# Kernel optimization log

Hardware: AMD Instinct MI355X
Metric: run time of the kernel (lower is better)

## Reference

```python
import jax, jax.numpy as jnp
import numpy as np

NUM_NODES = 16384
NUM_EDGES = 131072
NUM_MOLS = 512
H = 256          # hidden_dim
L = 3            # num_hidden_layers
NUM_RBF = 50
CUTOFF = 5.0
IN_DIM = 5
D_IN = IN_DIM + 3  # atom_types + spherical coords


def setup_inputs() -> dict:
    ks = jax.random.split(jax.random.key(0), 32)
    n = lambda k, s: jax.random.normal(k, s, dtype=jnp.float32) * 0.05
    return {
        "atom_types": jax.random.uniform(ks[0], (NUM_NODES, IN_DIM), dtype=jnp.float32),
        "coords_spherical": jax.random.normal(ks[1], (NUM_NODES, 3), dtype=jnp.float32),
        "edge_dist": jax.random.uniform(ks[2], (NUM_EDGES,), dtype=jnp.float32) * CUTOFF,
        "edge_index": jax.random.randint(ks[3], (2, NUM_EDGES), 0, NUM_NODES, dtype=jnp.int32),
        "node2mol": jnp.arange(NUM_NODES, dtype=jnp.int32) // (NUM_NODES // NUM_MOLS),
        "emb_Wm": n(ks[4], (D_IN, H)), "emb_bm": jnp.zeros((H,), jnp.float32),
        "emb_Wp": n(ks[5], (D_IN, H)), "emb_bp": jnp.zeros((H,), jnp.float32),
        "attn_Wqm": n(ks[6], (L, H, H)), "attn_Wkm": n(ks[7], (L, H, H)), "attn_Wvm": n(ks[8], (L, H, H)),
        "attn_Wqp": n(ks[9], (L, H, H)), "attn_Wkp": n(ks[10], (L, H, H)), "attn_Wvp": n(ks[11], (L, H, H)),
        "attn_We": n(ks[12], (L, NUM_RBF)), "attn_be": jnp.zeros((L,), jnp.float32),
        "mp_We": n(ks[13], (L, NUM_RBF, H)), "mp_be": jnp.zeros((L, H), jnp.float32),
        "mp_Wm": n(ks[14], (L, H, H)), "mp_bm": jnp.zeros((L, H), jnp.float32),
        "mp_Wp": n(ks[15], (L, H, H)), "mp_bp": jnp.zeros((L, H), jnp.float32),
        "ln_g": jnp.ones((L, H), jnp.float32), "ln_b": jnp.zeros((L, H), jnp.float32),
        "proj_W": n(ks[16], (H, H)), "proj_b": jnp.zeros((H,), jnp.float32),
        "head_W1": n(ks[17], (2 * H, H)), "head_b1": jnp.zeros((H,), jnp.float32),
        "head_W2": n(ks[18], (H, H // 2)), "head_b2": jnp.zeros((H // 2,), jnp.float32),
        "head_W3": n(ks[19], (H // 2, 1)), "head_b3": jnp.zeros((1,), jnp.float32),
    }


def _seg_softmax(s, seg, n):
    m = jax.ops.segment_max(s, seg, num_segments=n)
    e = jnp.exp(s - m[seg])
    z = jax.ops.segment_sum(e, seg, num_segments=n)
    return e / (z[seg] + 1e-9)


def _layernorm(x, g, b):
    mu = x.mean(-1, keepdims=True)
    v = ((x - mu) ** 2).mean(-1, keepdims=True)
    return (x - mu) * jax.lax.rsqrt(v + 1e-5) * g + b


def _forward(atom_types, coords_spherical, edge_dist,
             emb_Wm, emb_bm, emb_Wp, emb_bp,
             attn_Wqm, attn_Wkm, attn_Wvm, attn_Wqp, attn_Wkp, attn_Wvp, attn_We, attn_be,
             mp_We, mp_be, mp_Wm, mp_bm, mp_Wp, mp_bp,
             ln_g, ln_b, proj_W, proj_b,
             head_W1, head_b1, head_W2, head_b2, head_W3, head_b3,
             edge_index, node2mol):
    src, dst = edge_index[0], edge_index[1]
    N = NUM_NODES

    # --- RBF expansion (Schutt 2018): 50 gaussians on [0, cutoff] * cosine cutoff ---
    centers = jnp.linspace(0.0, CUTOFF, NUM_RBF)
    delta = CUTOFF / NUM_RBF
    env = 0.5 * (jnp.cos(jnp.pi * edge_dist / CUTOFF) + 1.0) * (edge_dist < CUTOFF)
    rbf = jnp.exp(-0.5 * ((edge_dist[:, None] - centers) / delta) ** 2) * env[:, None]  # [E, R]

    # --- Complex polar embedding ---
    x = jnp.concatenate([atom_types, coords_spherical], axis=-1)  # [N, 8]
    mag = jax.nn.softplus(x @ emb_Wm + emb_bm)
    ph = jnp.pi * jnp.tanh(x @ emb_Wp + emb_bp)

    for l in range(L):
        # --- Complex polar attention: |q||k| cos(phi_q - phi_k), edge bias from rbf ---
        qm, km, vm = mag @ attn_Wqm[l], mag @ attn_Wkm[l], mag @ attn_Wvm[l]
        qp, kp, vp = ph @ attn_Wqp[l], ph @ attn_Wkp[l], ph @ attn_Wvp[l]
        score = jnp.sum(qm[dst] * km[src] * jnp.cos(qp[dst] - kp[src]), axis=-1) / jnp.sqrt(float(H))
        score = score + rbf @ attn_We[l] + attn_be[l]          # [E]
        alpha = _seg_softmax(score, dst, N)                    # [E]
        new_mag = jax.ops.segment_sum(alpha[:, None] * vm[src], dst, num_segments=N)
        new_ph = jax.ops.segment_sum(alpha[:, None] * vp[src], dst, num_segments=N)

        # --- Complex message passing gated by RBF profile ---
        gate = jax.nn.silu(rbf @ mp_We[l] + mp_be[l])          # [E, H]
        agg_m = jax.ops.segment_sum(gate * new_mag[src], dst, num_segments=N)
        agg_p = jax.ops.segment_sum(gate * new_ph[src], dst, num_segments=N)
        new_mag = new_mag + agg_m @ mp_Wm[l] + mp_bm[l]
        new_ph = new_ph + agg_p @ mp_Wp[l] + mp_bp[l]

        # --- residual + LayerNorm on magnitude (dropout = identity at eval) ---
        new_mag = new_mag + mag
        new_ph = new_ph + ph
        mag = _layernorm(new_mag, ln_g[l], ln_b[l])
        ph = new_ph

    # --- real projection + dual (mean, sum) pooling per molecule ---
    atom_repr = (mag * jnp.cos(ph)) @ proj_W + proj_b          # [N, H]
    s = jax.ops.segment_sum(atom_repr, node2mol, num_segments=NUM_MOLS)
    cnt = jax.ops.segment_sum(jnp.ones((N, 1), atom_repr.dtype), node2mol, num_segments=NUM_MOLS)
    mol = jnp.concatenate([s / jnp.maximum(cnt, 1.0), s], axis=-1)  # [B, 2H]

    h = jax.nn.silu(mol @ head_W1 + head_b1)
    h = jax.nn.silu(h @ head_W2 + head_b2)
    return h @ head_W3 + head_b3                               # [B, 1]


def reference(atom_types, coords_spherical, edge_dist,
              emb_Wm, emb_bm, emb_Wp, emb_bp,
              attn_Wqm, attn_Wkm, attn_Wvm, attn_Wqp, attn_Wkp, attn_Wvp, attn_We, attn_be,
              mp_We, mp_be, mp_Wm, mp_bm, mp_Wp, mp_bp,
              ln_g, ln_b, proj_W, proj_b,
              head_W1, head_b1, head_W2, head_b2, head_W3, head_b3,
              edge_index, node2mol):
    return _forward(atom_types, coords_spherical, edge_dist,
                    emb_Wm, emb_bm, emb_Wp, emb_bp,
                    attn_Wqm, attn_Wkm, attn_Wvm, attn_Wqp, attn_Wkp, attn_Wvp, attn_We, attn_be,
                    mp_We, mp_be, mp_Wm, mp_bm, mp_Wp, mp_bp,
                    ln_g, ln_b, proj_W, proj_b,
                    head_W1, head_b1, head_W2, head_b2, head_W3, head_b3,
                    edge_index, node2mol)
```

## Files before the change

### kernel.cpp

```cpp
#include <hip/hip_runtime.h>
#include <math.h>

#define N_NODES 16384
#define N_EDGES 131072
#define N_MOLS 512
#define HDIM 256
#define NLAYER 3
#define NRBF 50
#define CUT 5.0f
#define HH (HDIM*HDIM)

typedef unsigned short u16;
typedef __attribute__((ext_vector_type(8))) short short8v;
typedef __attribute__((ext_vector_type(4))) float f32x4;
typedef __attribute__((ext_vector_type(4))) unsigned short u16x4;
typedef __attribute__((ext_vector_type(8))) unsigned short u16x8;
typedef __attribute__((ext_vector_type(2))) unsigned short u16x2;

__device__ __forceinline__ float softplusf(float x){ return fmaxf(x,0.f)+log1pf(expf(-fabsf(x))); }
__device__ __forceinline__ float siluf(float x){ return x/(1.f+expf(-x)); }
__device__ __forceinline__ float bf2f(u16 u){ union{unsigned int i; float f;}v; v.i=((unsigned int)u)<<16; return v.f; }
__device__ __forceinline__ u16 f2bf(float f){ union{float f; unsigned int i;}v; v.f=f; unsigned int r = v.i + 0x7FFFu + ((v.i>>16)&1u); return (u16)(r>>16); }

__device__ __forceinline__ void gload_lds16(const void* g, void* l){
  __builtin_amdgcn_global_load_lds((const __attribute__((address_space(1))) unsigned int*)g,
                                   (__attribute__((address_space(3))) unsigned int*)l, 16, 0, 0);
}

__global__ void k_hist(const int* __restrict__ dst, int* __restrict__ cnt){
  int e = blockIdx.x*256 + threadIdx.x;
  if(e < N_EDGES) atomicAdd(&cnt[dst[e]], 1);
}

__global__ __launch_bounds__(1024) void k_scan(const int* __restrict__ cnt,
                                               int* __restrict__ rowptr,
                                               int* __restrict__ cursor){
  __shared__ int part[1024];
  int tid = threadIdx.x;
  int base = tid*16;
  int loc[16]; int s=0;
  #pragma unroll
  for(int i=0;i<16;i++){ loc[i]=s; s+=cnt[base+i]; }
  part[tid]=s; __syncthreads();
  for(int off=1; off<1024; off<<=1){
    int v = (tid>=off)? part[tid-off] : 0;
    __syncthreads();
    part[tid] += v;
    __syncthreads();
  }
  int pre = (tid==0)?0:part[tid-1];
  #pragma unroll
  for(int i=0;i<16;i++){ int v = pre+loc[i]; rowptr[base+i]=v; cursor[base+i]=v; }
  if(tid==1023) rowptr[N_NODES]=part[1023];
}

__global__ void k_scatter(const int* __restrict__ dst, const int* __restrict__ src,
                          int* __restrict__ cursor,
                          int* __restrict__ perm, int* __restrict__ srcp){
  int e = blockIdx.x*256+threadIdx.x;
  if(e<N_EDGES){
    int p = atomicAdd(&cursor[dst[e]],1);
    perm[p]=e;
    srcp[p]=src[e];
  }
}

__global__ void k_rbf(const float* __restrict__ dist, const int* __restrict__ perm,
                      u16* __restrict__ rbfp){
  int gid = blockIdx.x*256+threadIdx.x;
  int i = gid>>6, r = gid&63;
  int e = perm[i];
  u16 o = 0;
  if(r<NRBF){
    float d = dist[e];
    float env = 0.5f*(cosf(3.14159265358979f*d/CUT)+1.f) * (d<CUT ? 1.f:0.f);
    float c = CUT*(float)r/(float)(NRBF-1);
    float u = (d - c)/(CUT/(float)NRBF);
    o = f2bf(expf(-0.5f*u*u)*env);
  }
  rbfp[(size_t)i*64+r] = o;
}

struct WDesc { const float* src; u16* dst; int K; int dK; };
struct WArgs { WDesc d[28]; };
__global__ __launch_bounds__(256) void k_wconv(WArgs a){
  WDesc w = a.d[blockIdx.x];
  int t = blockIdx.y;
  int ky = t >> 3, nx = t & 7;
  if(ky*32 >= w.dK) return;
  __shared__ float tile[32][33];
  int tid = threadIdx.x;
  int kk = tid >> 3, n4 = (tid & 7)*4;
  int k = ky*32 + kk;
  float4 v = {0.f,0.f,0.f,0.f};
  if(k < w.K) v = *(const float4*)(w.src + (size_t)k*HDIM + nx*32 + n4);
  tile[kk][n4+0]=v.x; tile[kk][n4+1]=v.y; tile[kk][n4+2]=v.z; tile[kk][n4+3]=v.w;
  __syncthreads();
  int nn = tid >> 3, k4 = (tid & 7)*4;
  u16x4 o;
  #pragma unroll
  for(int j=0;j<4;j++) o[j] = f2bf(tile[k4+j][nn]);
  *(u16x4*)(w.dst + (size_t)(nx*32+nn)*w.dK + ky*32 + k4) = o;
}

__global__ void k_embed(const float* __restrict__ at, const float* __restrict__ co,
                        const float* __restrict__ Wm, const float* __restrict__ bm,
                        const float* __restrict__ Wp, const float* __restrict__ bp,
                        float* __restrict__ mag, float* __restrict__ ph,
                        u16* __restrict__ magb, u16* __restrict__ phb){
  int n = blockIdx.x; int h = threadIdx.x;
  __shared__ float x[8];
  if(threadIdx.x<5) x[threadIdx.x] = at[n*5+threadIdx.x];
  else if(threadIdx.x<8) x[threadIdx.x] = co[n*3+threadIdx.x-5];
  __syncthreads();
  float tm=bm[h], tp=bp[h];
  #pragma unroll
  for(int i=0;i<8;i++){ tm = fmaf(x[i],Wm[i*HDIM+h],tm); tp = fmaf(x[i],Wp[i*HDIM+h],tp); }
  size_t idx = (size_t)n*HDIM+h;
  float m = softplusf(tm);
  float p = 3.14159265358979f*tanhf(tp);
  mag[idx]=m; ph[idx]=p; magb[idx]=f2bf(m); phb[idx]=f2bf(p);
}

template<int MODE>
__device__ __forceinline__ void gemm_body(const u16* __restrict__ A,
                                          const u16* __restrict__ Bt,
                                          const float* __restrict__ bias,
                                          void* __restrict__ outp, int K, int ostr){
  __shared__ __align__(16) u16 As[128*64];
  __shared__ __align__(16) u16 Bs[64*64];
  int tid = threadIdx.x;
  int lane = tid & 63, wid = tid >> 6;
  int wm = wid & 1, wn = wid >> 1;
  int m0 = blockIdx.y * 128;
  int n0 = blockIdx.x * 64;
  const size_t Kb = (size_t)K*2;
  f32x4 acc[4][2] = {};
  for(int k0=0; k0<K; k0+=64){
    #pragma unroll
    for(int it=0; it<4; it++){
      int off = it*4096 + tid*16;
      int row = off >> 7, col = off & 127;
      const char* g = (const char*)A + (size_t)(m0+row)*Kb + (size_t)k0*2 + col;
      gload_lds16(g, (char*)As + it*4096 + wid*1024);
    }
    #pragma unroll
    for(int it=0; it<2; it++){
      int off = it*4096 + tid*16;
      int row = off >> 7, col = off & 127;
      const char* g = (const char*)Bt + (size_t)(n0+row)*Kb + (size_t)k0*2 + col;
      gload_lds16(g, (char*)Bs + it*4096 + wid*1024);
    }
    __syncthreads();
    #pragma unroll
    for(int ks=0; ks<2; ks++){
      int kl = ks*32 + (lane>>4)*8;
      short8v a[4], b[2];
      #pragma unroll
      for(int fm=0; fm<4; fm++){
        int m = wm*64 + fm*16 + (lane&15);
        a[fm] = *(const short8v*)&As[m*64 + kl];
      }
      #pragma unroll
      for(int fn=0; fn<2; fn++){
        int n = wn*32 + fn*16 + (lane&15);
        b[fn] = *(const short8v*)&Bs[n*64 + kl];
      }
      #pragma unroll
      for(int fm=0; fm<4; fm++)
        #pragma unroll
        for(int fn=0; fn<2; fn++)
          acc[fm][fn] = __builtin_amdgcn_mfma_f32_16x16x32_bf16(a[fm], b[fn], acc[fm][fn], 0,0,0);
    }
    __syncthreads();
  }
  int ro = (lane>>4)*4, co = lane&15;
  #pragma unroll
  for(int fm=0; fm<4; fm++){
    #pragma unroll
    for(int fn=0; fn<2; fn++){
      int col = n0 + wn*32 + fn*16 + co;
      float bv = bias ? bias[col] : 0.f;
      #pragma unroll
      for(int r=0; r<4; r++){
        int row = m0 + wm*64 + fm*16 + ro + r;
        float v = acc[fm][fn][r] + bv;
        size_t ci = (size_t)row*ostr + col;
        if(MODE==1) ((u16*)outp)[ci] = f2bf(siluf(v));
        else if(MODE==2) ((float*)outp)[ci] += v;
        else ((float*)outp)[ci] = v;
      }
    }
  }
}

struct Qkv2Args { const u16* Wm[3]; const u16* Wp[3]; u16* qpk; u16* kvpk; };
__global__ __launch_bounds__(256,2) void k_gemm_qkv2(const u16* __restrict__ magb,
                                                     const u16* __restrict__ phb,
                                                     Qkv2Args a){
  __shared__ __align__(16) u16 Am[128*64];
  __shared__ __align__(16) u16 Ap[128*64];
  __shared__ __align__(16) u16 Bm[64*64];
  __shared__ __align__(16) u16 Bp[64*64];
  int z = blockIdx.z;
  const u16* Wmz = a.Wm[z];
  const u16* Wpz = a.Wp[z];
  int tid = threadIdx.x;
  int lane = tid & 63, wid = tid >> 6;
  int wm = wid & 1, wn = wid >> 1;
  int m0 = blockIdx.y * 128;
  int n0 = blockIdx.x * 64;
  const size_t Kb = 512;
  f32x4 accm[4][2] = {}, accp[4][2] = {};
  for(int k0=0; k0<256; k0+=64){
    #pragma unroll
    for(int it=0; it<4; it++){
      int off = it*4096 + tid*16;
      int row = off >> 7, col = off & 127;
      size_t go = (size_t)(m0+row)*Kb + (size_t)k0*2 + col;
      gload_lds16((const char*)magb + go, (char*)Am + it*4096 + wid*1024);
      gload_lds16((const char*)phb  + go, (char*)Ap + it*4096 + wid*1024);
    }
    #pragma unroll
    for(int it=0; it<2; it++){
      int off = it*4096 + tid*16;
      int row = off >> 7, col = off & 127;
      size_t go = (size_t)(n0+row)*Kb + (size_t)k0*2 + col;
      gload_lds16((const char*)Wmz + go, (char*)Bm + it*4096 + wid*1024);
      gload_lds16((const char*)Wpz + go, (char*)Bp + it*4096 + wid*1024);
    }
    __syncthreads();
    #pragma unroll
    for(int ks=0; ks<2; ks++){
      int kl = ks*32 + (lane>>4)*8;
      short8v am[4], ap[4], bm_[2], bp_[2];
      #pragma unroll
      for(int fm=0; fm<4; fm++){
        int m = wm*64 + fm*16 + (lane&15);
        am[fm] = *(const short8v*)&Am[m*64 + kl];
        ap[fm] = *(const short8v*)&Ap[m*64 + kl];
      }
      #pragma unroll
      for(int fn=0; fn<2; fn++){
        int n = wn*32 + fn*16 + (lane&15);
        bm_[fn] = *(const short8v*)&Bm[n*64 + kl];
        bp_[fn] = *(const short8v*)&Bp[n*64 + kl];
      }
      #pragma unroll
      for(int fm=0; fm<4; fm++)
        #pragma unroll
        for(int fn=0; fn<2; fn++){
          accm[fm][fn] = __builtin_amdgcn_mfma_f32_16x16x32_bf16(am[fm], bm_[fn], accm[fm][fn], 0,0,0);
          accp[fm][fn] = __builtin_amdgcn_mfma_f32_16x16x32_bf16(ap[fm], bp_[fn], accp[fm][fn], 0,0,0);
        }
    }
    __syncthreads();
  }
  int ro = (lane>>4)*4, co = lane&15;
  #pragma unroll
  for(int fm=0; fm<4; fm++){
    #pragma unroll
    for(int fn=0; fn<2; fn++){
      int col = n0 + wn*32 + fn*16 + co;
      #pragma unroll
      for(int r=0; r<4; r++){
        int row = m0 + wm*64 + fm*16 + ro + r;
        float mv = accm[fm][fn][r];
        float pv = accp[fm][fn][r];
        u16 o0, o1;
        if(z<2){
          float sn, cs;
          __sincosf(pv, &sn, &cs);
          o0 = f2bf(mv*cs); o1 = f2bf(mv*sn);
        } else {
          o0 = f2bf(mv); o1 = f2bf(pv);
        }
        u16* base = (z==0) ? (a.qpk + (size_t)row*512)
                           : (a.kvpk + (size_t)row*1024 + (z==2 ? 512 : 0));
        base[col] = o0;
        base[col+256] = o1;
      }
    }
  }
}

__global__ __launch_bounds__(256,2) void k_gemm_gate(const u16* __restrict__ rbfp,
                                                     const u16* __restrict__ Wt,
                                                     const float* __restrict__ be,
                                                     u16* __restrict__ gate){
  gemm_body<1>(rbfp, Wt, be, gate, 64, 256);
}
struct MpArgs { const u16* A[2]; const u16* Wt[2]; const float* b[2]; float* C[2]; };
__global__ __launch_bounds__(256,2) void k_gemm_mp(MpArgs a){
  int z = blockIdx.z;
  gemm_body<2>(a.A[z], a.Wt[z], a.b[z], a.C[z], HDIM, 256);
}
__global__ __launch_bounds__(256,2) void k_gemm_proj(const u16* __restrict__ Ab,
                                                     const u16* __restrict__ Wt,
                                                     const float* __restrict__ b,
                                                     float* __restrict__ C){
  gemm_body<3>(Ab, Wt, b, C, HDIM, 256);
}

__global__ __launch_bounds__(256) void k_attn_fused(
    const int* __restrict__ rowptr, const int* __restrict__ srcp,
    const u16* __restrict__ qpack, const u16* __restrict__ kvpack,
    const u16* __restrict__ rbfp,
    const float* __restrict__ We, const float* __restrict__ be,
    float* __restrict__ nmag, float* __restrict__ nph,
    u16* __restrict__ npack)
{
  int wid = threadIdx.x >> 6, lane = threadIdx.x & 63;
  int hid = lane >> 5, l = lane & 31;
  int d = blockIdx.x*4 + wid;
  int b = rowptr[d], e = rowptr[d+1];
  const u16* qb = qpack + (size_t)d*512 + l*8;
  u16x8 qc8 = *(const u16x8*)qb;
  u16x8 qs8 = *(const u16x8*)(qb + 256);
  float qcf[8], qsf[8];
  #pragma unroll
  for(int j=0;j<8;j++){ qcf[j]=bf2f(qc8[j]); qsf[j]=bf2f(qs8[j]); }
  float We0 = (2*l   < NRBF) ? We[2*l]   : 0.f;
  float We1 = (2*l+1 < NRBF) ? We[2*l+1] : 0.f;
  float be0 = be[0];
  float z = 0.f;
  float avm[8] = {0,0,0,0,0,0,0,0}, avp[8] = {0,0,0,0,0,0,0,0};
  for(int i = b + hid; i < e; i += 2){
    int s = srcp[i];
    const u16* kb = kvpack + (size_t)s*1024 + l*8;
    u16x8 kc8 = *(const u16x8*)kb;
    u16x8 ks8 = *(const u16x8*)(kb + 256);
    u16x8 vm8 = *(const u16x8*)(kb + 512);
    u16x8 vp8 = *(const u16x8*)(kb + 768);
    u16x2 rb2 = *(const u16x2*)(rbfp + (size_t)i*64 + 2*l);
    float p = 0.f;
    #pragma unroll
    for(int j=0;j<8;j++){
      p = fmaf(qcf[j], bf2f(kc8[j]), p);
      p = fmaf(qsf[j], bf2f(ks8[j]), p);
    }
    float t = fmaf(bf2f(rb2[0]), We0, fmaf(bf2f(rb2[1]), We1, p*0.0625f));
    #pragma unroll
    for(int off=16; off; off>>=1) t += __shfl_xor(t, off, 64);
    float w = __expf(t + be0);
    z += w;
    #pragma unroll
    for(int j=0;j<8;j++){
      avm[j] = fmaf(w, bf2f(vm8[j]), avm[j]);
      avp[j] = fmaf(w, bf2f(vp8[j]), avp[j]);
    }
  }
  z += __shfl_xor(z, 32, 64);
  #pragma unroll
  for(int j=0;j<8;j++){
    avm[j] += __shfl_xor(avm[j], 32, 64);
    avp[j] += __shfl_xor(avp[j], 32, 64);
  }
  if(hid==0){
    float inv = 1.f/(z + 1e-9f);
    u16x8 mb, pb;
    #pragma unroll
    for(int j=0;j<8;j++){ avm[j]*=inv; avp[j]*=inv; mb[j]=f2bf(avm[j]); pb[j]=f2bf(avp[j]); }
    size_t no = (size_t)d*256 + l*8;
    *(float4*)(nmag + no)     = make_float4(avm[0],avm[1],avm[2],avm[3]);
    *(float4*)(nmag + no + 4) = make_float4(avm[4],avm[5],avm[6],avm[7]);
    *(float4*)(nph + no)      = make_float4(avp[0],avp[1],avp[2],avp[3]);
    *(float4*)(nph + no + 4)  = make_float4(avp[4],avp[5],avp[6],avp[7]);
    u16* nb = npack + (size_t)d*512 + l*8;
    *(u16x8*)nb = mb;
    *(u16x8*)(nb + 256) = pb;
  }
}

__global__ __launch_bounds__(256) void k_mp_agg(const int* __restrict__ rowptr,
                         const int* __restrict__ srcp, const u16* __restrict__ gate,
                         const u16* __restrict__ npack,
                         u16* __restrict__ aggm, u16* __restrict__ aggp){
  int wid = threadIdx.x >> 6, lane = threadIdx.x & 63;
  int hid = lane >> 5, l = lane & 31;
  int n = blockIdx.x*4 + wid;
  int b = rowptr[n], e = rowptr[n+1];
  float am[8] = {0,0,0,0,0,0,0,0}, ap[8] = {0,0,0,0,0,0,0,0};
  for(int i = b + hid; i < e; i += 2){
    int s = srcp[i];
    u16x8 g8 = *(const u16x8*)(gate + (size_t)i*256 + l*8);
    const u16* nb = npack + (size_t)s*512 + l*8;
    u16x8 m8 = *(const u16x8*)nb;
    u16x8 p8 = *(const u16x8*)(nb + 256);
    #pragma unroll
    for(int j=0;j<8;j++){
      float g = bf2f(g8[j]);
      am[j] = fmaf(g, bf2f(m8[j]), am[j]);
      ap[j] = fmaf(g, bf2f(p8[j]), ap[j]);
    }
  }
  #pragma unroll
  for(int j=0;j<8;j++){
    am[j] += __shfl_xor(am[j], 32, 64);
    ap[j] += __shfl_xor(ap[j], 32, 64);
  }
  if(hid==0){
    u16x8 amb, apb;
    #pragma unroll
    for(int j=0;j<8;j++){ amb[j]=f2bf(am[j]); apb[j]=f2bf(ap[j]); }
    size_t o = (size_t)n*256 + l*8;
    *(u16x8*)(aggm + o) = amb;
    *(u16x8*)(aggp + o) = apb;
  }
}

template<int LAST>
__global__ __launch_bounds__(256) void k_resid_ln(const float* __restrict__ nmag, const float* __restrict__ nph,
                           float* __restrict__ mag, float* __restrict__ ph,
                           u16* __restrict__ magb, u16* __restrict__ phb,
                           u16* __restrict__ tcosb,
                           const float* __restrict__ g, const float* __restrict__ b){
  int n = blockIdx.x, tid = threadIdx.x;
  size_t idx = (size_t)n*HDIM+tid;
  float t = nmag[idx] + mag[idx];
  float s1=t, s2=t*t;
  #pragma unroll
  for(int off=32; off; off>>=1){ s1 += __shfl_down(s1,off,64); s2 += __shfl_down(s2,off,64); }
  __shared__ float w1[4], w2[4], bc[2];
  int wid = tid>>6, lane = tid&63;
  if(lane==0){ w1[wid]=s1; w2[wid]=s2; }
  __syncthreads();
  if(tid==0){
    float a=w1[0]+w1[1]+w1[2]+w1[3];
    float q=w2[0]+w2[1]+w2[2]+w2[3];
    float mu = a*(1.f/HDIM);
    float var = q*(1.f/HDIM) - mu*mu;
    bc[0]=mu; bc[1]=rsqrtf(var+1e-5f);
  }
  __syncthreads();
  float mu=bc[0], rs=bc[1];
  float ln = (t-mu)*rs*g[tid]+b[tid];
  float p2 = nph[idx] + ph[idx];
  if(LAST){
    tcosb[idx] = f2bf(ln*__cosf(p2));
  } else {
    mag[idx] = ln; magb[idx] = f2bf(ln);
    ph[idx] = p2; phb[idx] = f2bf(p2);
  }
}

__global__ void k_pool(const float* __restrict__ arepr, const int* __restrict__ n2m,
                       float* __restrict__ spool, float* __restrict__ cntf){
  int gid = blockIdx.x*256+threadIdx.x;
  int n = gid>>8, h = gid&255;
  int m = n2m[n];
  atomicAdd(&spool[(size_t)m*HDIM+h], arepr[(size_t)n*HDIM+h]);
  if(h==0) atomicAdd(&cntf[m], 1.f);
}

__global__ __launch_bounds__(256) void k_head(const float* __restrict__ spool, const float* __restrict__ cntf,
                       const float* __restrict__ W1, const float* __restrict__ b1,
                       const float* __restrict__ W2, const float* __restrict__ b2,
                       const float* __restrict__ W3, const float* __restrict__ b3,
                       float* __restrict__ out){
  __shared__ float smol[2*HDIM];
  __shared__ float sh1[HDIM];
  __shared__ float sh2[HDIM/2];
  int m = blockIdx.x, tid = threadIdx.x;
  float sv = spool[(size_t)m*HDIM+tid];
  float c = cntf[m];
  smol[tid] = sv/fmaxf(c,1.f);
  smol[HDIM+tid] = sv;
  __syncthreads();
  float a = b1[tid];
  for(int i=0;i<2*HDIM;i++) a = fmaf(smol[i], W1[i*HDIM+tid], a);
  sh1[tid] = siluf(a);
  __syncthreads();
  if(tid<128){
    float a2 = b2[tid];
    for(int i=0;i<HDIM;i++) a2 = fmaf(sh1[i], W2[i*128+tid], a2);
    sh2[tid] = siluf(a2);
  }
  __syncthreads();
  if(tid<64){
    float p = sh2[tid]*W3[tid] + sh2[tid+64]*W3[tid+64];
    #pragma unroll
    for(int off=32; off; off>>=1) p += __shfl_down(p,off,64);
    if(tid==0) out[m] = p + b3[0];
  }
}

extern "C" void kernel_launch(void* const* d_in, const int* in_sizes, int n_in,
                              void* d_out, int out_size, void* d_ws, size_t ws_size,
                              hipStream_t stream){
  const float* atom_types = (const float*)d_in[0];
  const float* coords     = (const float*)d_in[1];
  const float* edge_dist  = (const float*)d_in[2];
  const int*   edge_index = (const int*)d_in[3];
  const int*   node2mol   = (const int*)d_in[4];
  const float* emb_Wm = (const float*)d_in[5];
  const float* emb_bm = (const float*)d_in[6];
  const float* emb_Wp = (const float*)d_in[7];
  const float* emb_bp = (const float*)d_in[8];
  const float* attn_Wqm = (const float*)d_in[9];
  const float* attn_Wkm = (const float*)d_in[10];
  const float* attn_Wvm = (const float*)d_in[11];
  const float* attn_Wqp = (const float*)d_in[12];
  const float* attn_Wkp = (const float*)d_in[13];
  const float* attn_Wvp = (const float*)d_in[14];
  const float* attn_We  = (const float*)d_in[15];
  const float* attn_be  = (const float*)d_in[16];
  const float* mp_We = (const float*)d_in[17];
  const float* mp_be = (const float*)d_in[18];
  const float* mp_Wm = (const float*)d_in[19];
  const float* mp_bm = (const float*)d_in[20];
  const float* mp_Wp = (const float*)d_in[21];
  const float* mp_bp = (const float*)d_in[22];
  const float* ln_g = (const float*)d_in[23];
  const float* ln_b = (const float*)d_in[24];
  const float* proj_W = (const float*)d_in[25];
  const float* proj_b = (const float*)d_in[26];
  const float* head_W1 = (const float*)d_in[27];
  const float* head_b1 = (const float*)d_in[28];
  const float* head_W2 = (const float*)d_in[29];
  const float* head_b2 = (const float*)d_in[30];
  const float* head_W3 = (const float*)d_in[31];
  const float* head_b3 = (const float*)d_in[32];
  float* out = (float*)d_out;

  float* ws = (float*)d_ws;
  const size_t NH = (size_t)N_NODES*HDIM;
  size_t o = 0;
  float* mag = ws + o; o += NH;
  float* ph  = ws + o; o += NH;
  float* nmag= ws + o; o += NH;
  float* nph = ws + o; o += NH;
  float* spool = ws + o; o += (size_t)N_MOLS*HDIM;
  float* cntf  = ws + o; o += N_MOLS;
  int* rowptr = (int*)(ws + o); o += N_NODES+1;
  int* cnt    = (int*)(ws + o); o += N_NODES;
  int* cursor = (int*)(ws + o); o += N_NODES;
  int* perm   = (int*)(ws + o); o += N_EDGES;
  int* srcp   = (int*)(ws + o); o += N_EDGES + 1;
  u16* magb = (u16*)(ws + o); o += NH/2;
  u16* phb  = (u16*)(ws + o); o += NH/2;
  u16* aggmb= (u16*)(ws + o); o += NH/2;
  u16* aggpb= (u16*)(ws + o); o += NH/2;
  u16* npack= (u16*)(ws + o); o += NH;
  u16* rbfp = (u16*)(ws + o); o += (size_t)N_EDGES*32;
  u16* qpack= (u16*)(ws + o); o += NH;
  u16* kvpack=(u16*)(ws + o); o += 2*NH;
  o += NH;
  u16* wt   = (u16*)(ws + o); o += (25*(size_t)HH + 3*HDIM*64)/2;
  u16* gatep = qpack;
  float* arepr = nmag;
  u16* tcosb = aggmb;

  const int* src = edge_index;
  const int* dst = edge_index + N_EDGES;

  WArgs wa;
  for(int l=0;l<NLAYER;l++){
    const float* srcs[6] = {attn_Wqm+(size_t)l*HH, attn_Wkm+(size_t)l*HH, attn_Wvm+(size_t)l*HH,
                            attn_Wqp+(size_t)l*HH, attn_Wkp+(size_t)l*HH, attn_Wvp+(size_t)l*HH};
    for(int j=0;j<6;j++){ wa.d[l*6+j] = { srcs[j], wt + (size_t)(l*6+j)*HH, HDIM, HDIM }; }
    wa.d[18+l] = { mp_Wm+(size_t)l*HH, wt + (size_t)(18+l)*HH, HDIM, HDIM };
    wa.d[21+l] = { mp_Wp+(size_t)l*HH, wt + (size_t)(21+l)*HH, HDIM, HDIM };
    wa.d[25+l] = { mp_We+(size_t)l*NRBF*HDIM, wt + (size_t)25*HH + (size_t)l*HDIM*64, NRBF, 64 };
  }
  wa.d[24] = { proj_W, wt + (size_t)24*HH, HDIM, HDIM };

  hipMemsetAsync(cnt, 0, N_NODES*sizeof(int), stream);
  k_hist<<<N_EDGES/256,256,0,stream>>>(dst, cnt);
  k_scan<<<1,1024,0,stream>>>(cnt, rowptr, cursor);
  k_scatter<<<N_EDGES/256,256,0,stream>>>(dst, src, cursor, perm, srcp);
  k_wconv<<<dim3(28,64),256,0,stream>>>(wa);
  k_rbf<<<(N_EDGES*64)/256,256,0,stream>>>(edge_dist, perm, rbfp);
  k_embed<<<N_NODES,256,0,stream>>>(atom_types, coords, emb_Wm, emb_bm, emb_Wp, emb_bp,
                                    mag, ph, magb, phb);

  dim3 gn(HDIM/64, N_NODES/128);
  dim3 ge(HDIM/64, N_EDGES/128);
  for(int l=0;l<NLAYER;l++){
    Qkv2Args qa;
    qa.Wm[0] = wt + (size_t)(l*6+0)*HH;
    qa.Wm[1] = wt + (size_t)(l*6+1)*HH;
    qa.Wm[2] = wt + (size_t)(l*6+2)*HH;
    qa.Wp[0] = wt + (size_t)(l*6+3)*HH;
    qa.Wp[1] = wt + (size_t)(l*6+4)*HH;
    qa.Wp[2] = wt + (size_t)(l*6+5)*HH;
    qa.qpk = qpack; qa.kvpk = kvpack;
    k_gemm_qkv2<<<dim3(4,128,3),256,0,stream>>>(magb, phb, qa);
    k_attn_fused<<<N_NODES/4,256,0,stream>>>(rowptr, srcp, qpack, kvpack,
                                             rbfp, attn_We+(size_t)l*NRBF, attn_be+l,
                                             nmag, nph, npack);
    k_gemm_gate<<<ge,256,0,stream>>>(rbfp, wt + (size_t)25*HH + (size_t)l*HDIM*64,
                                     mp_be+(size_t)l*HDIM, gatep);
    k_mp_agg<<<N_NODES/4,256,0,stream>>>(rowptr, srcp, gatep, npack, aggmb, aggpb);
    MpArgs ma;
    ma.A[0]=aggmb; ma.A[1]=aggpb;
    ma.Wt[0]=wt + (size_t)(18+l)*HH; ma.Wt[1]=wt + (size_t)(21+l)*HH;
    ma.b[0]=mp_bm+(size_t)l*HDIM; ma.b[1]=mp_bp+(size_t)l*HDIM;
    ma.C[0]=nmag; ma.C[1]=nph;
    k_gemm_mp<<<dim3(4,128,2),256,0,stream>>>(ma);
    if(l < NLAYER-1)
      k_resid_ln<0><<<N_NODES,256,0,stream>>>(nmag, nph, mag, ph, magb, phb, nullptr,
                                              ln_g+(size_t)l*HDIM, ln_b+(size_t)l*HDIM);
    else
      k_resid_ln<1><<<N_NODES,256,0,stream>>>(nmag, nph, mag, ph, magb, phb, tcosb,
                                              ln_g+(size_t)l*HDIM, ln_b+(size_t)l*HDIM);
  }
  k_gemm_proj<<<gn,256,0,stream>>>(tcosb, wt + (size_t)24*HH, proj_b, arepr);
  hipMemsetAsync(spool, 0, ((size_t)N_MOLS*HDIM+N_MOLS)*sizeof(float), stream);
  k_pool<<<NH/256,256,0,stream>>>(arepr, node2mol, spool, cntf);
  k_head<<<N_MOLS,256,0,stream>>>(spool, cntf, head_W1, head_b1, head_W2, head_b2, head_W3, head_b3, out);
}
```

Measured before the change: 956.1 us.

## Use full-width N tiles with XOR-swizzled LDS in all dense GEMMs

All dense GEMMs (qkv, gate, message-passing and projection) now have each 512-thread block compute a 128x256 output tile covering the whole N dimension. The A tile is loaded once per block instead of once per 64-column slice. Global-to-LDS chunk placement is XOR-swizzled by row so the MFMA fragment reads avoid LDS bank conflicts. The trade-off is far fewer blocks (384 for qkv, 256 for mp, 128 for proj), more LDS per block (96KB in qkv) and more accumulator registers, so occupancy and load balance across CUs may suffer.

New measurement: 855.1 us. -10.6%, faster.

```diff
diff --git a/kernel.cpp b/kernel.cpp
--- a/kernel.cpp
+++ b/kernel.cpp
@@ -123,69 +123,71 @@
 }
 
 template<int MODE>
-__device__ __forceinline__ void gemm_body(const u16* __restrict__ A,
-                                          const u16* __restrict__ Bt,
-                                          const float* __restrict__ bias,
-                                          void* __restrict__ outp, int K, int ostr){
+__device__ __forceinline__ void gemm_fullN(const u16* __restrict__ A,
+                                           const u16* __restrict__ Bt,
+                                           const float* __restrict__ bias,
+                                           void* __restrict__ outp, int K){
   __shared__ __align__(16) u16 As[128*64];
-  __shared__ __align__(16) u16 Bs[64*64];
+  __shared__ __align__(16) u16 Bs[256*64];
   int tid = threadIdx.x;
   int lane = tid & 63, wid = tid >> 6;
   int wm = wid & 1, wn = wid >> 1;
   int m0 = blockIdx.y * 128;
-  int n0 = blockIdx.x * 64;
   const size_t Kb = (size_t)K*2;
-  f32x4 acc[4][2] = {};
-  for(int k0=0; k0<K; k0+=64){
+  f32x4 acc[4][4] = {};
+  for(int k0=0;k0<K;k0+=64){
+    #pragma unroll
+    for(int it=0; it<2; it++){
+      int ci = it*512 + tid;
+      int row = ci>>3, cl = ci&7;
+      int csw = cl ^ (row&7);
+      size_t go = (size_t)(m0+row)*Kb + (size_t)k0*2 + csw*16;
+      gload_lds16((const char*)A+go, (char*)As + it*8192 + wid*1024);
+    }
     #pragma unroll
     for(int it=0; it<4; it++){
-      int off = it*4096 + tid*16;
-      int row = off >> 7, col = off & 127;
-      const char* g = (const char*)A + (size_t)(m0+row)*Kb + (size_t)k0*2 + col;
-      gload_lds16(g, (char*)As + it*4096 + wid*1024);
-    }
-    #pragma unroll
-    for(int it=0; it<2; it++){
-      int off = it*4096 + tid*16;
-      int row = off >> 7, col = off & 127;
-      const char* g = (const char*)Bt + (size_t)(n0+row)*Kb + (size_t)k0*2 + col;
-      gload_lds16(g, (char*)Bs + it*4096 + wid*1024);
+      int ci = it*512 + tid;
+      int row = ci>>3, cl = ci&7;
+      int csw = cl ^ (row&7);
+      size_t go = (size_t)row*Kb + (size_t)k0*2 + csw*16;
+      gload_lds16((const char*)Bt+go, (char*)Bs + it*8192 + wid*1024);
     }
     __syncthreads();
     #pragma unroll
-    for(int ks=0; ks<2; ks++){
-      int kl = ks*32 + (lane>>4)*8;
-      short8v a[4], b[2];
-      #pragma unroll
-      for(int fm=0; fm<4; fm++){
+    for(int ks=0;ks<2;ks++){
+      short8v a[4], b[4];
+      #pragma unroll
+      for(int fm=0;fm<4;fm++){
         int m = wm*64 + fm*16 + (lane&15);
-        a[fm] = *(const short8v*)&As[m*64 + kl];
+        int ch = (ks*4 + (lane>>4)) ^ (m&7);
+        a[fm] = *(const short8v*)&As[m*64 + ch*8];
       }
       #pragma unroll
-      for(int fn=0; fn<2; fn++){
-        int n = wn*32 + fn*16 + (lane&15);
-        b[fn] = *(const short8v*)&Bs[n*64 + kl];
+      for(int fn=0;fn<4;fn++){
+        int n = wn*64 + fn*16 + (lane&15);
+        int ch = (ks*4 + (lane>>4)) ^ (n&7);
+        b[fn] = *(const short8v*)&Bs[n*64 + ch*8];
       }
       #pragma unroll
-      for(int fm=0; fm<4; fm++)
+      for(int fm=0;fm<4;fm++)
         #pragma unroll
-        for(int fn=0; fn<2; fn++)
-          acc[fm][fn] = __builtin_amdgcn_mfma_f32_16x16x32_bf16(a[fm], b[fn], acc[fm][fn], 0,0,0);
+        for(int fn=0;fn<4;fn++)
+          acc[fm][fn] = __builtin_amdgcn_mfma_f32_16x16x32_bf16(a[fm], b[fn], acc[fm][fn],0,0,0);
     }
     __syncthreads();
   }
-  int ro = (lane>>4)*4, co = lane&15;
-  #pragma unroll
-  for(int fm=0; fm<4; fm++){
-    #pragma unroll
-    for(int fn=0; fn<2; fn++){
-      int col = n0 + wn*32 + fn*16 + co;
+  int ro=(lane>>4)*4, co=lane&15;
+  #pragma unroll
+  for(int fm=0;fm<4;fm++){
+    #pragma unroll
+    for(int fn=0;fn<4;fn++){
+      int col = wn*64 + fn*16 + co;
       float bv = bias ? bias[col] : 0.f;
       #pragma unroll
-      for(int r=0; r<4; r++){
+      for(int r=0;r<4;r++){
         int row = m0 + wm*64 + fm*16 + ro + r;
         float v = acc[fm][fn][r] + bv;
-        size_t ci = (size_t)row*ostr + col;
+        size_t ci = (size_t)row*256 + col;
         if(MODE==1) ((u16*)outp)[ci] = f2bf(siluf(v));
         else if(MODE==2) ((float*)outp)[ci] += v;
         else ((float*)outp)[ci] = v;
@@ -194,14 +196,32 @@
   }
 }
 
-struct Qkv2Args { const u16* Wm[3]; const u16* Wp[3]; u16* qpk; u16* kvpk; };
-__global__ __launch_bounds__(256,2) void k_gemm_qkv2(const u16* __restrict__ magb,
-                                                     const u16* __restrict__ phb,
-                                                     Qkv2Args a){
-  __shared__ __align__(16) u16 Am[128*64];
-  __shared__ __align__(16) u16 Ap[128*64];
-  __shared__ __align__(16) u16 Bm[64*64];
-  __shared__ __align__(16) u16 Bp[64*64];
+__global__ __launch_bounds__(512) void k_gemm_gate(const u16* __restrict__ rbfp,
+                                                   const u16* __restrict__ Wt,
+                                                   const float* __restrict__ be,
+                                                   u16* __restrict__ gate){
+  gemm_fullN<1>(rbfp, Wt, be, gate, 64);
+}
+struct MpArgs { const u16* A[2]; const u16* Wt[2]; const float* b[2]; float* C[2]; };
+__global__ __launch_bounds__(512) void k_gemm_mp(MpArgs a){
+  int z = blockIdx.z;
+  gemm_fullN<2>(a.A[z], a.Wt[z], a.b[z], a.C[z], HDIM);
+}
+__global__ __launch_bounds__(512) void k_gemm_proj(const u16* __restrict__ Ab,
+                                                   const u16* __restrict__ Wt,
+                                                   const float* __restrict__ b,
+                                                   float* __restrict__ C){
+  gemm_fullN<3>(Ab, Wt, b, C, HDIM);
+}
+
+struct Qkv3Args { const u16* Wm[3]; const u16* Wp[3]; u16* qpk; u16* kvpk; };
+__global__ __launch_bounds__(512) void k_gemm_qkv3(const u16* __restrict__ magb,
+                                                   const u16* __restrict__ phb,
+                                                   Qkv3Args a){
+  __shared__ __align__(16) u16 Ams[128*64];
+  __shared__ __align__(16) u16 Aps[128*64];
+  __shared__ __align__(16) u16 Bms[256*64];
+  __shared__ __align__(16) u16 Bps[256*64];
   int z = blockIdx.z;
   const u16* Wmz = a.Wm[z];
   const u16* Wpz = a.Wp[z];
@@ -209,61 +229,63 @@
   int lane = tid & 63, wid = tid >> 6;
   int wm = wid & 1, wn = wid >> 1;
   int m0 = blockIdx.y * 128;
-  int n0 = blockIdx.x * 64;
   const size_t Kb = 512;
-  f32x4 accm[4][2] = {}, accp[4][2] = {};
-  for(int k0=0; k0<256; k0+=64){
+  f32x4 accm[4][4] = {}, accp[4][4] = {};
+  for(int k0=0;k0<256;k0+=64){
+    #pragma unroll
+    for(int it=0; it<2; it++){
+      int ci = it*512 + tid;
+      int row = ci>>3, cl = ci&7;
+      int csw = cl ^ (row&7);
+      size_t go = (size_t)(m0+row)*Kb + (size_t)k0*2 + csw*16;
+      gload_lds16((const char*)magb+go, (char*)Ams + it*8192 + wid*1024);
+      gload_lds16((const char*)phb +go, (char*)Aps + it*8192 + wid*1024);
+    }
     #pragma unroll
     for(int it=0; it<4; it++){
-      int off = it*4096 + tid*16;
-      int row = off >> 7, col = off & 127;
-      size_t go = (size_t)(m0+row)*Kb + (size_t)k0*2 + col;
-      gload_lds16((const char*)magb + go, (char*)Am + it*4096 + wid*1024);
-      gload_lds16((const char*)phb  + go, (char*)Ap + it*4096 + wid*1024);
-    }
-    #pragma unroll
-    for(int it=0; it<2; it++){
-      int off = it*4096 + tid*16;
-      int row = off >> 7, col = off & 127;
-      size_t go = (size_t)(n0+row)*Kb + (size_t)k0*2 + col;
-      gload_lds16((const char*)Wmz + go, (char*)Bm + it*4096 + wid*1024);
-      gload_lds16((const char*)Wpz + go, (char*)Bp + it*4096 + wid*1024);
+      int ci = it*512 + tid;
+      int row = ci>>3, cl = ci&7;
+      int csw = cl ^ (row&7);
+      size_t go = (size_t)row*Kb + (size_t)k0*2 + csw*16;
+      gload_lds16((const char*)Wmz+go, (char*)Bms + it*8192 + wid*1024);
+      gload_lds16((const char*)Wpz+go, (char*)Bps + it*8192 + wid*1024);
     }
     __syncthreads();
     #pragma unroll
-    for(int ks=0; ks<2; ks++){
-      int kl = ks*32 + (lane>>4)*8;
-      short8v am[4], ap[4], bm_[2], bp_[2];
-      #pragma unroll
-      for(int fm=0; fm<4; fm++){
+    for(int ks=0;ks<2;ks++){
+      short8v am[4], ap[4], bm_[4], bp_[4];
+      #pragma unroll
+      for(int fm=0;fm<4;fm++){
         int m = wm*64 + fm*16 + (lane&15);
-        am[fm] = *(const short8v*)&Am[m*64 + kl];
-        ap[fm] = *(const short8v*)&Ap[m*64 + kl];
+        int ch = (ks*4 + (lane>>4)) ^ (m&7);
+        am[fm] = *(const short8v*)&Ams[m*64 + ch*8];
+        ap[fm] = *(const short8v*)&Aps[m*64 + ch*8];
       }
       #pragma unroll
-      for(int fn=0; fn<2; fn++){
-        int n = wn*32 + fn*16 + (lane&15);
-        bm_[fn] = *(const short8v*)&Bm[n*64 + kl];
-        bp_[fn] = *(const short8v*)&Bp[n*64 + kl];
+      for(int fn=0;fn<4;fn++){
+        int n = wn*64 + fn*16 + (lane&15);
+        int ch = (ks*4 + (lane>>4)) ^ (n&7);
+        bm_[fn] = *(const short8v*)&Bms[n*64 + ch*8];
+        bp_[fn] = *(const short8v*)&Bps[n*64 + ch*8];
       }
       #pragma unroll
-      for(int fm=0; fm<4; fm++)
+      for(int fm=0;fm<4;fm++)
         #pragma unroll
-        for(int fn=0; fn<2; fn++){
-          accm[fm][fn] = __builtin_amdgcn_mfma_f32_16x16x32_bf16(am[fm], bm_[fn], accm[fm][fn], 0,0,0);
-          accp[fm][fn] = __builtin_amdgcn_mfma_f32_16x16x32_bf16(ap[fm], bp_[fn], accp[fm][fn], 0,0,0);
+        for(int fn=0;fn<4;fn++){
+          accm[fm][fn] = __builtin_amdgcn_mfma_f32_16x16x32_bf16(am[fm], bm_[fn], accm[fm][fn],0,0,0);
+          accp[fm][fn] = __builtin_amdgcn_mfma_f32_16x16x32_bf16(ap[fm], bp_[fn], accp[fm][fn],0,0,0);
         }
     }
     __syncthreads();
   }
-  int ro = (lane>>4)*4, co = lane&15;
-  #pragma unroll
-  for(int fm=0; fm<4; fm++){
-    #pragma unroll
-    for(int fn=0; fn<2; fn++){
-      int col = n0 + wn*32 + fn*16 + co;
-      #pragma unroll
-      for(int r=0; r<4; r++){
+  int ro=(lane>>4)*4, co=lane&15;
+  #pragma unroll
+  for(int fm=0;fm<4;fm++){
+    #pragma unroll
+    for(int fn=0;fn<4;fn++){
+      int col = wn*64 + fn*16 + co;
+      #pragma unroll
+      for(int r=0;r<4;r++){
         int row = m0 + wm*64 + fm*16 + ro + r;
         float mv = accm[fm][fn][r];
         float pv = accp[fm][fn][r];
@@ -282,24 +304,6 @@
       }
     }
   }
-}
-
-__global__ __launch_bounds__(256,2) void k_gemm_gate(const u16* __restrict__ rbfp,
-                                                     const u16* __restrict__ Wt,
-                                                     const float* __restrict__ be,
-                                                     u16* __restrict__ gate){
-  gemm_body<1>(rbfp, Wt, be, gate, 64, 256);
-}
-struct MpArgs { const u16* A[2]; const u16* Wt[2]; const float* b[2]; float* C[2]; };
-__global__ __launch_bounds__(256,2) void k_gemm_mp(MpArgs a){
-  int z = blockIdx.z;
-  gemm_body<2>(a.A[z], a.Wt[z], a.b[z], a.C[z], HDIM, 256);
-}
-__global__ __launch_bounds__(256,2) void k_gemm_proj(const u16* __restrict__ Ab,
-                                                     const u16* __restrict__ Wt,
-                                                     const float* __restrict__ b,
-                                                     float* __restrict__ C){
-  gemm_body<3>(Ab, Wt, b, C, HDIM, 256);
 }
 
 __global__ __launch_bounds__(256) void k_attn_fused(
@@ -574,10 +578,8 @@
   k_embed<<<N_NODES,256,0,stream>>>(atom_types, coords, emb_Wm, emb_bm, emb_Wp, emb_bp,
                                     mag, ph, magb, phb);
 
-  dim3 gn(HDIM/64, N_NODES/128);
-  dim3 ge(HDIM/64, N_EDGES/128);
   for(int l=0;l<NLAYER;l++){
-    Qkv2Args qa;
+    Qkv3Args qa;
     qa.Wm[0] = wt + (size_t)(l*6+0)*HH;
     qa.Wm[1] = wt + (size_t)(l*6+1)*HH;
     qa.Wm[2] = wt + (size_t)(l*6+2)*HH;
@@ -585,19 +587,19 @@
     qa.Wp[1] = wt + (size_t)(l*6+4)*HH;
     qa.Wp[2] = wt + (size_t)(l*6+5)*HH;
     qa.qpk = qpack; qa.kvpk = kvpack;
-    k_gemm_qkv2<<<dim3(4,128,3),256,0,stream>>>(magb, phb, qa);
+    k_gemm_qkv3<<<dim3(1,N_NODES/128,3),512,0,stream>>>(magb, phb, qa);
     k_attn_fused<<<N_NODES/4,256,0,stream>>>(rowptr, srcp, qpack, kvpack,
                                              rbfp, attn_We+(size_t)l*NRBF, attn_be+l,
                                              nmag, nph, npack);
-    k_gemm_gate<<<ge,256,0,stream>>>(rbfp, wt + (size_t)25*HH + (size_t)l*HDIM*64,
-                                     mp_be+(size_t)l*HDIM, gatep);
+    k_gemm_gate<<<dim3(1,N_EDGES/128),512,0,stream>>>(rbfp, wt + (size_t)25*HH + (size_t)l*HDIM*64,
+                                                      mp_be+(size_t)l*HDIM, gatep);
     k_mp_agg<<<N_NODES/4,256,0,stream>>>(rowptr, srcp, gatep, npack, aggmb, aggpb);
     MpArgs ma;
     ma.A[0]=aggmb; ma.A[1]=aggpb;
     ma.Wt[0]=wt + (size_t)(18+l)*HH; ma.Wt[1]=wt + (size_t)(21+l)*HH;
     ma.b[0]=mp_bm+(size_t)l*HDIM; ma.b[1]=mp_bp+(size_t)l*HDIM;
     ma.C[0]=nmag; ma.C[1]=nph;
-    k_gemm_mp<<<dim3(4,128,2),256,0,stream>>>(ma);
+    k_gemm_mp<<<dim3(1,N_NODES/128,2),512,0,stream>>>(ma);
     if(l < NLAYER-1)
       k_resid_ln<0><<<N_NODES,256,0,stream>>>(nmag, nph, mag, ph, magb, phb, nullptr,
                                               ln_g+(size_t)l*HDIM, ln_b+(size_t)l*HDIM);
@@ -605,7 +607,7 @@
       k_resid_ln<1><<<N_NODES,256,0,stream>>>(nmag, nph, mag, ph, magb, phb, tcosb,
                                               ln_g+(size_t)l*HDIM, ln_b+(size_t)l*HDIM);
   }
-  k_gemm_proj<<<gn,256,0,stream>>>(tcosb, wt + (size_t)24*HH, proj_b, arepr);
+  k_gemm_proj<<<dim3(1,N_NODES/128),512,0,stream>>>(tcosb, wt + (size_t)24*HH, proj_b, arepr);
   hipMemsetAsync(spool, 0, ((size_t)N_MOLS*HDIM+N_MOLS)*sizeof(float), stream);
   k_pool<<<NH/256,256,0,stream>>>(arepr, node2mol, spool, cntf);
   k_head<<<N_MOLS,256,0,stream>>>(spool, cntf, head_W1, head_b1, head_W2, head_b2, head_W3, head_b3, out);
```
